# Kernel tuning notes

Measured on AMD Instinct MI355X. Metric: run time of the kernel, lower is better.

The kernel has to match this reference:

```python
import jax, jax.numpy as jnp
import numpy as np

GRID = 24          # sqrt(576)
MM = 1024          # mm_hidden_size
HID = 4096         # hidden_size
HEADS = 8          # mm_hidden_size // 128
NQ = GRID * GRID   # 576 queries / tokens
BATCH = 16
K = 2              # top-k == num_experts == 2


def _sincos_1d(d, pos):
    omega = np.arange(d // 2, dtype=np.float32) / (d / 2.0)
    omega = 1.0 / 10000 ** omega
    out = np.einsum('m,d->md', pos.reshape(-1).astype(np.float32), omega)
    return np.concatenate([np.sin(out), np.cos(out)], axis=1)


def _sincos_2d(d, g):
    gw, gh = np.meshgrid(np.arange(g, dtype=np.float32), np.arange(g, dtype=np.float32))
    return np.concatenate([_sincos_1d(d // 2, gh), _sincos_1d(d // 2, gw)], axis=1)


def layer_norm(x, g, b, eps=1e-5):
    mu = x.mean(-1, keepdims=True)
    var = ((x - mu) ** 2).mean(-1, keepdims=True)
    return (x - mu) * jax.lax.rsqrt(var + eps) * g + b


def mha(q, k, v, Wi, bi, Wo, bo, H):
    # q,k,v: [N, S, D]; Wi: [3D, D]; torch nn.MultiheadAttention semantics
    N, S, D = q.shape
    dh = D // H
    Wq, Wk, Wv = Wi[:D], Wi[D:2 * D], Wi[2 * D:]
    bq, bk, bv = bi[:D], bi[D:2 * D], bi[2 * D:]
    qp = (q @ Wq.T + bq).reshape(N, S, H, dh)
    kp = (k @ Wk.T + bk).reshape(N, -1, H, dh)
    vp = (v @ Wv.T + bv).reshape(N, -1, H, dh)
    scale = jnp.asarray(1.0 / np.sqrt(dh), q.dtype)
    scores = jnp.einsum('bqhd,bkhd->bhqk', qp, kp) * scale
    attn = jax.nn.softmax(scores, axis=-1)
    out = jnp.einsum('bhqk,bkhd->bqhd', attn, vp).reshape(N, S, D)
    return out @ Wo.T + bo


def _gating(xf, w_gate, w_noise, noise):
    # noisy top-k gating, training mode, k == num_experts == 2
    clean = xf @ w_gate                               # [B, 2]
    std = jax.nn.softplus(xf @ w_noise) + 0.01
    logits = jax.nn.softmax(clean + noise * std, axis=1)
    top_vals, top_idx = jax.lax.top_k(logits, K)      # min(k+1, n) == 2
    gates_k = top_vals / (top_vals.sum(1, keepdims=True) + 1e-6)
    rows = jnp.arange(xf.shape[0])[:, None]
    return jnp.zeros_like(logits).at[rows, top_idx].set(gates_k)


def setup_inputs() -> dict:
    key = jax.random.key(0)
    ks = jax.random.split(key, 10)
    s = 0.02
    f32 = jnp.float32
    return dict(
        x=jax.random.normal(ks[0], (BATCH, NQ, MM), f32),
        noise=jax.random.normal(ks[1], (BATCH * NQ, 2), f32),
        W1=jax.random.normal(ks[2], (HID, MM), f32) * s,
        b1=jnp.zeros((HID,), f32),
        W2=jax.random.normal(ks[3], (HID, HID), f32) * s,
        b2=jnp.zeros((HID,), f32),
        query=jax.random.normal(ks[4], (NQ, MM), f32) * s,
        pos_embed=jnp.asarray(_sincos_2d(MM, GRID), f32),
        ln_q_g=jnp.ones((MM,), f32), ln_q_b=jnp.zeros((MM,), f32),
        ln_kv_g=jnp.ones((MM,), f32), ln_kv_b=jnp.zeros((MM,), f32),
        in_proj_w=jax.random.normal(ks[5], (3 * MM, MM), f32) * s,
        in_proj_b=jnp.zeros((3 * MM,), f32),
        out_w=jax.random.normal(ks[6], (MM, MM), f32) * s,
        out_b=jnp.zeros((MM,), f32),
        w_gate=jax.random.normal(ks[7], (MM, 2), f32) * s,
        w_noise=jax.random.normal(ks[8], (MM, 2), f32) * s,
    )


def reference(x, noise, W1, b1, W2, b2, query, pos_embed, ln_q_g, ln_q_b,
              ln_kv_g, ln_kv_b, in_proj_w, in_proj_b, out_w, out_b,
              w_gate, w_noise):
    N, C, D = x.shape

    def projection(t):  # Linear -> GELU(exact) -> Linear
        h = jax.nn.gelu(t @ W1.T + b1, approximate=False)
        return h @ W2.T + b2

    # --- Resampler expert (kv_proj/ln_post/proj are identity here) ---
    kv = layer_norm(x, ln_kv_g, ln_kv_b)                    # [N, 576, D]
    q = layer_norm(query, ln_q_g, ln_q_b) + pos_embed       # [576, D]
    q = jnp.broadcast_to(q, (N, C, D))
    attn_out = mha(q, kv + pos_embed, kv, in_proj_w, in_proj_b, out_w, out_b, HEADS)

    e0 = projection(x)          # expert 0: MLP projection
    e1 = projection(attn_out)   # expert 1: resampler then projection

    gates = _gating(x.reshape(N * C, D), w_gate, w_noise, noise).reshape(N, C, 2)
    # stack(...,-1) @ gates[...,None] squeezed == gated sum over experts
    return e0 * gates[..., 0:1] + e1 * gates[..., 1:2]
```

## Files before the change

### kernel.cpp

```cpp
#include <hip/hip_runtime.h>
#include <hip/hip_bf16.h>
#include <cstdint>
#include <cstddef>

typedef __bf16 bf16;
typedef __bf16 bf16x4 __attribute__((ext_vector_type(4)));
typedef __bf16 bf16x8 __attribute__((ext_vector_type(8)));
typedef float  f32x4  __attribute__((ext_vector_type(4)));

#define BATCH 16
#define NQ    576
#define MM    1024
#define HID   4096
#define HEADS 8
#define DH    128
#define ROWS  (BATCH*NQ)

typedef const unsigned int __attribute__((address_space(1)))* gas_ptr;
typedef unsigned int __attribute__((address_space(3)))* las_ptr;

__device__ __forceinline__ void async16(const bf16* g, bf16* l) {
  __builtin_amdgcn_global_load_lds((gas_ptr)g, (las_ptr)l, 16, 0, 0);
}

__global__ __launch_bounds__(256) void cvt_kernel(
    const float* __restrict__ s, bf16* __restrict__ d)
{
  const int i = (blockIdx.x * 256 + threadIdx.x) * 4;
  f32x4 v = *(const f32x4*)(s + i);
  bf16x4 o;
#pragma unroll
  for (int j = 0; j < 4; ++j) o[j] = (bf16)v[j];
  *(bf16x4*)(d + i) = o;
}

enum { MODE_BIAS = 0, MODE_GG = 1, MODE_GGACC = 2, MODE_GB = 3 };

template <int MODE, typename OutT>
__global__ __launch_bounds__(256) void gemm_bt(
    const bf16* __restrict__ A, const bf16* __restrict__ W,
    const float* __restrict__ bias, OutT* __restrict__ C,
    const float* __restrict__ gates, int M, int N, int K)
{
  __shared__ bf16 As[128 * 32];
  __shared__ bf16 Bs[128 * 32];

  const int tid  = threadIdx.x;
  const int lane = tid & 63;
  const int w    = tid >> 6;
  const int wm   = (w & 1) * 64;
  const int wn   = (w >> 1) * 64;
  const int l15  = lane & 15;
  const int quad = lane >> 4;
  const int m0   = blockIdx.y * 128;
  const int n0   = blockIdx.x * 128;

  f32x4 acc[4][4] = {};

  int ar0 = m0 + (tid >> 2);      if (ar0 > M - 1) ar0 = M - 1;
  int ar1 = m0 + 64 + (tid >> 2); if (ar1 > M - 1) ar1 = M - 1;
  const int kc = (tid & 3) * 8;
  const bf16* ap0 = A + (size_t)ar0 * K + kc;
  const bf16* ap1 = A + (size_t)ar1 * K + kc;
  const bf16* bp0 = W + (size_t)(n0 + (tid >> 2)) * K + kc;
  const bf16* bp1 = W + (size_t)(n0 + 64 + (tid >> 2)) * K + kc;
  bf16* lA0 = As + tid * 8;
  bf16* lA1 = As + 2048 + tid * 8;
  bf16* lB0 = Bs + tid * 8;
  bf16* lB1 = Bs + 2048 + tid * 8;

  const int ko = quad * 8;

  for (int kt = 0; kt < K; kt += 32) {
    async16(ap0 + kt, lA0);
    async16(ap1 + kt, lA1);
    async16(bp0 + kt, lB0);
    async16(bp1 + kt, lB1);
    __syncthreads();

    bf16x8 af[4], bfr[4];
#pragma unroll
    for (int i = 0; i < 4; ++i)
      af[i] = *(const bf16x8*)(As + (wm + i * 16 + l15) * 32 + ko);
#pragma unroll
    for (int i = 0; i < 4; ++i)
      bfr[i] = *(const bf16x8*)(Bs + (wn + i * 16 + l15) * 32 + ko);
#pragma unroll
    for (int mi = 0; mi < 4; ++mi)
#pragma unroll
      for (int ni = 0; ni < 4; ++ni)
        acc[mi][ni] = __builtin_amdgcn_mfma_f32_16x16x32_bf16(
            af[mi], bfr[ni], acc[mi][ni], 0, 0, 0);
    __syncthreads();
  }

#pragma unroll
  for (int ni = 0; ni < 4; ++ni) {
    const int col = n0 + wn + ni * 16 + l15;
    const float bv = bias[col];
#pragma unroll
    for (int mi = 0; mi < 4; ++mi) {
      const int rowb = m0 + wm + mi * 16 + quad * 4;
#pragma unroll
      for (int r = 0; r < 4; ++r) {
        const int gr = rowb + r;
        if (gr < M) {
          const size_t idx = (size_t)gr * N + col;
          if (MODE == MODE_GB) {
            C[idx] = (OutT)(acc[mi][ni][r] +
                            (gates[gr * 2] + gates[gr * 2 + 1]) * bv);
          } else {
            float v = acc[mi][ni][r] + bv;
            if (MODE == MODE_GG || MODE == MODE_GGACC)
              v = 0.5f * v * (1.0f + erff(v * 0.70710678118654752f));
            if (MODE == MODE_GG)
              C[idx] = (OutT)(v * gates[gr * 2]);
            else if (MODE == MODE_GGACC)
              C[idx] = (OutT)((float)C[idx] + v * gates[gr * 2 + 1]);
            else
              C[idx] = (OutT)v;
          }
        }
      }
    }
  }
}

__global__ __launch_bounds__(256) void attn_kernel(
    const bf16* __restrict__ qp, const bf16* __restrict__ kp,
    const bf16* __restrict__ vp, bf16* __restrict__ ctx)
{
  __shared__ bf16 Qs[64 * 128];
  __shared__ bf16 Ks[64 * 128];
  __shared__ bf16 Vt[128 * 64];
  __shared__ bf16 Ps[64 * 64];

  const int qt = blockIdx.x, b = blockIdx.y, h = blockIdx.z;
  const int tid = threadIdx.x, lane = tid & 63, w = tid >> 6;
  const int l15 = lane & 15, quad = lane >> 4;
  const int q0 = qt * 64;

#pragma unroll
  for (int i = 0; i < 4; ++i) {
    const int c = i * 256 + tid;
    const int row = c >> 4, col = (c & 15) * 8;
    *(bf16x8*)(Qs + row * 128 + col) =
        *(const bf16x8*)(qp + (size_t)(q0 + row) * MM + h * DH + col);
  }

  float m_r[4], l_r[4];
  f32x4 accO[8] = {};
#pragma unroll
  for (int r = 0; r < 4; ++r) { m_r[r] = -1e30f; l_r[r] = 0.f; }

  const float scale = 0.08838834764831843f;

  for (int kt = 0; kt < 9; ++kt) {
    __syncthreads();
    const int kbase = b * NQ + kt * 64;
#pragma unroll
    for (int i = 0; i < 4; ++i) {
      const int c = i * 256 + tid;
      const int row = c >> 4, col = (c & 15) * 8;
      *(bf16x8*)(Ks + row * 128 + col) =
          *(const bf16x8*)(kp + (size_t)(kbase + row) * MM + h * DH + col);
      bf16x8 vv = *(const bf16x8*)(vp + (size_t)(kbase + row) * MM + h * DH + col);
#pragma unroll
      for (int j = 0; j < 8; ++j) Vt[(col + j) * 64 + row] = vv[j];
    }
    __syncthreads();

    f32x4 sacc[4] = {};
#pragma unroll
    for (int kcq = 0; kcq < 4; ++kcq) {
      bf16x8 aq = *(const bf16x8*)(Qs + (w * 16 + l15) * 128 + kcq * 32 + quad * 8);
#pragma unroll
      for (int ni = 0; ni < 4; ++ni) {
        bf16x8 bk = *(const bf16x8*)(Ks + (ni * 16 + l15) * 128 + kcq * 32 + quad * 8);
        sacc[ni] = __builtin_amdgcn_mfma_f32_16x16x32_bf16(aq, bk, sacc[ni], 0, 0, 0);
      }
    }
#pragma unroll
    for (int ni = 0; ni < 4; ++ni)
#pragma unroll
      for (int r = 0; r < 4; ++r) sacc[ni][r] *= scale;

    float p[4][4];
#pragma unroll
    for (int r = 0; r < 4; ++r) {
      float mx = fmaxf(fmaxf(sacc[0][r], sacc[1][r]), fmaxf(sacc[2][r], sacc[3][r]));
#pragma unroll
      for (int off = 8; off >= 1; off >>= 1) mx = fmaxf(mx, __shfl_xor(mx, off, 64));
      const float mnew = fmaxf(m_r[r], mx);
      const float al = expf(m_r[r] - mnew);
      float rs = 0.f;
#pragma unroll
      for (int ni = 0; ni < 4; ++ni) { p[ni][r] = expf(sacc[ni][r] - mnew); rs += p[ni][r]; }
#pragma unroll
      for (int off = 8; off >= 1; off >>= 1) rs += __shfl_xor(rs, off, 64);
      l_r[r] = l_r[r] * al + rs;
      m_r[r] = mnew;
#pragma unroll
      for (int ni2 = 0; ni2 < 8; ++ni2) accO[ni2][r] *= al;
    }

#pragma unroll
    for (int ni = 0; ni < 4; ++ni)
#pragma unroll
      for (int r = 0; r < 4; ++r)
        Ps[(w * 16 + quad * 4 + r) * 64 + ni * 16 + l15] = (bf16)p[ni][r];

#pragma unroll
    for (int kc2 = 0; kc2 < 2; ++kc2) {
      bf16x8 ap = *(const bf16x8*)(Ps + (w * 16 + l15) * 64 + kc2 * 32 + quad * 8);
#pragma unroll
      for (int ni2 = 0; ni2 < 8; ++ni2) {
        bf16x8 bv = *(const bf16x8*)(Vt + (ni2 * 16 + l15) * 64 + kc2 * 32 + quad * 8);
        accO[ni2] = __builtin_amdgcn_mfma_f32_16x16x32_bf16(ap, bv, accO[ni2], 0, 0, 0);
      }
    }
  }

#pragma unroll
  for (int r = 0; r < 4; ++r) {
    const float inv = 1.0f / l_r[r];
    const int qrow = q0 + w * 16 + quad * 4 + r;
#pragma unroll
    for (int ni2 = 0; ni2 < 8; ++ni2)
      ctx[(size_t)(b * NQ + qrow) * MM + h * DH + ni2 * 16 + l15] =
          (bf16)(accO[ni2][r] * inv);
  }
}

__global__ __launch_bounds__(256) void ln_kv_kernel(
    const float* __restrict__ x, const float* __restrict__ g,
    const float* __restrict__ bta, const float* __restrict__ pos,
    bf16* __restrict__ kv, bf16* __restrict__ kin)
{
  const int row = blockIdx.x, tid = threadIdx.x;
  f32x4 xv = *(const f32x4*)(x + (size_t)row * MM + tid * 4);
  float s = 0.f, ss = 0.f;
#pragma unroll
  for (int j = 0; j < 4; ++j) { s += xv[j]; ss += xv[j] * xv[j]; }
#pragma unroll
  for (int off = 32; off >= 1; off >>= 1) { s += __shfl_xor(s, off, 64); ss += __shfl_xor(ss, off, 64); }
  __shared__ float red[8];
  const int w = tid >> 6;
  if ((tid & 63) == 0) { red[w] = s; red[4 + w] = ss; }
  __syncthreads();
  s  = red[0] + red[1] + red[2] + red[3];
  ss = red[4] + red[5] + red[6] + red[7];
  const float mu = s * (1.0f / MM);
  const float rsig = rsqrtf(ss * (1.0f / MM) - mu * mu + 1e-5f);
  const int prow = row % NQ;
#pragma unroll
  for (int j = 0; j < 4; ++j) {
    const int c = tid * 4 + j;
    const float y = (xv[j] - mu) * rsig * g[c] + bta[c];
    kv[(size_t)row * MM + c]  = (bf16)y;
    kin[(size_t)row * MM + c] = (bf16)(y + pos[(size_t)prow * MM + c]);
  }
}

__global__ __launch_bounds__(256) void ln_q_kernel(
    const float* __restrict__ query, const float* __restrict__ g,
    const float* __restrict__ bta, const float* __restrict__ pos,
    bf16* __restrict__ qout)
{
  const int row = blockIdx.x, tid = threadIdx.x;
  f32x4 xv = *(const f32x4*)(query + (size_t)row * MM + tid * 4);
  float s = 0.f, ss = 0.f;
#pragma unroll
  for (int j = 0; j < 4; ++j) { s += xv[j]; ss += xv[j] * xv[j]; }
#pragma unroll
  for (int off = 32; off >= 1; off >>= 1) { s += __shfl_xor(s, off, 64); ss += __shfl_xor(ss, off, 64); }
  __shared__ float red[8];
  const int w = tid >> 6;
  if ((tid & 63) == 0) { red[w] = s; red[4 + w] = ss; }
  __syncthreads();
  s  = red[0] + red[1] + red[2] + red[3];
  ss = red[4] + red[5] + red[6] + red[7];
  const float mu = s * (1.0f / MM);
  const float rsig = rsqrtf(ss * (1.0f / MM) - mu * mu + 1e-5f);
#pragma unroll
  for (int j = 0; j < 4; ++j) {
    const int c = tid * 4 + j;
    const float y = (xv[j] - mu) * rsig * g[c] + bta[c] + pos[(size_t)row * MM + c];
    qout[(size_t)row * MM + c] = (bf16)y;
  }
}

__global__ __launch_bounds__(256) void gating_kernel(
    const float* __restrict__ x, const float* __restrict__ wg,
    const float* __restrict__ wn, const float* __restrict__ noise,
    float* __restrict__ gates)
{
  const int row = blockIdx.x, tid = threadIdx.x;
  f32x4 xv = *(const f32x4*)(x + (size_t)row * MM + tid * 4);
  float a0 = 0, a1 = 0, c0 = 0, c1 = 0;
#pragma unroll
  for (int j = 0; j < 4; ++j) {
    const int c = tid * 4 + j;
    a0 += xv[j] * wg[c * 2];
    a1 += xv[j] * wg[c * 2 + 1];
    c0 += xv[j] * wn[c * 2];
    c1 += xv[j] * wn[c * 2 + 1];
  }
#pragma unroll
  for (int off = 32; off >= 1; off >>= 1) {
    a0 += __shfl_xor(a0, off, 64); a1 += __shfl_xor(a1, off, 64);
    c0 += __shfl_xor(c0, off, 64); c1 += __shfl_xor(c1, off, 64);
  }
  __shared__ float red[16];
  const int w = tid >> 6;
  if ((tid & 63) == 0) { red[w * 4] = a0; red[w * 4 + 1] = a1; red[w * 4 + 2] = c0; red[w * 4 + 3] = c1; }
  __syncthreads();
  if (tid == 0) {
    a0 = red[0] + red[4] + red[8] + red[12];
    a1 = red[1] + red[5] + red[9] + red[13];
    c0 = red[2] + red[6] + red[10] + red[14];
    c1 = red[3] + red[7] + red[11] + red[15];
    const float sp0 = fmaxf(c0, 0.f) + log1pf(expf(-fabsf(c0)));
    const float sp1 = fmaxf(c1, 0.f) + log1pf(expf(-fabsf(c1)));
    const float l0 = a0 + noise[row * 2]     * (sp0 + 0.01f);
    const float l1 = a1 + noise[row * 2 + 1] * (sp1 + 0.01f);
    const float mx = fmaxf(l0, l1);
    const float e0 = expf(l0 - mx), e1 = expf(l1 - mx);
    const float inv = 1.0f / (e0 + e1);
    const float p0 = e0 * inv, p1 = e1 * inv;
    const float den = 1.0f / (p0 + p1 + 1e-6f);
    gates[row * 2]     = p0 * den;
    gates[row * 2 + 1] = p1 * den;
  }
}

extern "C" void kernel_launch(void* const* d_in, const int* in_sizes, int n_in,
                              void* d_out, int out_size, void* d_ws, size_t ws_size,
                              hipStream_t stream)
{
  const float* x       = (const float*)d_in[0];
  const float* noise   = (const float*)d_in[1];
  const float* W1      = (const float*)d_in[2];
  const float* b1      = (const float*)d_in[3];
  const float* W2      = (const float*)d_in[4];
  const float* b2      = (const float*)d_in[5];
  const float* query   = (const float*)d_in[6];
  const float* pos     = (const float*)d_in[7];
  const float* ln_q_g  = (const float*)d_in[8];
  const float* ln_q_b  = (const float*)d_in[9];
  const float* ln_kv_g = (const float*)d_in[10];
  const float* ln_kv_b = (const float*)d_in[11];
  const float* ipw     = (const float*)d_in[12];
  const float* ipb     = (const float*)d_in[13];
  const float* out_w   = (const float*)d_in[14];
  const float* out_b   = (const float*)d_in[15];
  const float* w_gate  = (const float*)d_in[16];
  const float* w_noise = (const float*)d_in[17];
  float* out = (float*)d_out;

  char* ws = (char*)d_ws;
  bf16*  kin   = (bf16*)(ws);
  bf16*  ctx   = kin;
  bf16*  kp    = (bf16*)(ws + 18874368);
  bf16*  vp    = (bf16*)(ws + 37748736);
  bf16*  qbuf  = (bf16*)(ws + 56623104);
  bf16*  qp    = (bf16*)(ws + 57802752);
  bf16*  ipwb  = (bf16*)(ws + 58982400);
  bf16*  outwb = (bf16*)(ws + 65273856);
  bf16*  h     = (bf16*)(ws);
  bf16*  x_bf  = (bf16*)(ws + 75497472);
  bf16*  W1b   = (bf16*)(ws + 94371840);
  bf16*  W2b   = (bf16*)(ws + 102760448);
  float* gates = (float*)(ws + 136314880);
  bf16*  kv       = (bf16*)d_out;
  bf16*  attn_out = (bf16*)((char*)d_out + 18874368);

  gating_kernel<<<ROWS, 256, 0, stream>>>(x, w_gate, w_noise, noise, gates);
  cvt_kernel<<<9216,  256, 0, stream>>>(x,  x_bf);
  cvt_kernel<<<4096,  256, 0, stream>>>(W1, W1b);
  cvt_kernel<<<16384, 256, 0, stream>>>(W2, W2b);
  cvt_kernel<<<3072,  256, 0, stream>>>(ipw,   ipwb);
  cvt_kernel<<<1024,  256, 0, stream>>>(out_w, outwb);

  ln_kv_kernel<<<ROWS, 256, 0, stream>>>(x, ln_kv_g, ln_kv_b, pos, kv, kin);
  ln_q_kernel<<<NQ, 256, 0, stream>>>(query, ln_q_g, ln_q_b, pos, qbuf);

  gemm_bt<MODE_BIAS, bf16><<<dim3(8, 5),  256, 0, stream>>>(qbuf, ipwb, ipb, qp, nullptr, NQ, MM, MM);
  gemm_bt<MODE_BIAS, bf16><<<dim3(8, 72), 256, 0, stream>>>(kin, ipwb + (size_t)MM * MM, ipb + MM, kp, nullptr, ROWS, MM, MM);
  gemm_bt<MODE_BIAS, bf16><<<dim3(8, 72), 256, 0, stream>>>(kv, ipwb + (size_t)2 * MM * MM, ipb + 2 * MM, vp, nullptr, ROWS, MM, MM);

  attn_kernel<<<dim3(9, BATCH, HEADS), 256, 0, stream>>>(qp, kp, vp, ctx);

  gemm_bt<MODE_BIAS, bf16><<<dim3(8, 72), 256, 0, stream>>>(ctx, outwb, out_b, attn_out, nullptr, ROWS, MM, MM);

  gemm_bt<MODE_GG,    bf16><<<dim3(32, 72), 256, 0, stream>>>(x_bf,     W1b, b1, h, gates, ROWS, HID, MM);
  gemm_bt<MODE_GGACC, bf16><<<dim3(32, 72), 256, 0, stream>>>(attn_out, W1b, b1, h, gates, ROWS, HID, MM);
  gemm_bt<MODE_GB,   float><<<dim3(32, 72), 256, 0, stream>>>(h,        W2b, b2, out, gates, ROWS, HID, HID);
}
```

Before: 1.413 ms.

## Add 256x256-tile triple-buffered GEMM kernel for the large projection GEMMs

Adds a new 512-thread GEMM kernel with 256x256 output tiles and a three-stage async global-to-LDS pipeline with XOR-swizzled shared memory. It also remaps workgroups in a swizzled order for cache locality and raises MFMA wave priority around the compute sections. The three large W1/W2 GEMMs now use it, while the old kernel is reduced to bias-only mode. The larger tiles are meant to raise arithmetic intensity and overlap loads with MFMA work, at the cost of more registers and LDS per block, lower occupancy, and no bounds checks, so M and N must be multiples of 256.

```diff
diff --git a/kernel.cpp b/kernel.cpp
--- a/kernel.cpp
+++ b/kernel.cpp
@@ -35,6 +35,143 @@
 }
 
 enum { MODE_BIAS = 0, MODE_GG = 1, MODE_GGACC = 2, MODE_GB = 3 };
+
+template <int MODE, typename OutT>
+__global__ __launch_bounds__(512) void gemm_big(
+    const bf16* __restrict__ A, const bf16* __restrict__ W,
+    const float* __restrict__ bias, OutT* __restrict__ C,
+    const float* __restrict__ gates, int M, int N, int K)
+{
+  __shared__ char LDS[3 * 32768];
+
+  const int tid  = threadIdx.x;
+  const int lane = tid & 63;
+  const int w    = tid >> 6;
+  const int w_m  = w >> 2;
+  const int w_n  = w & 3;
+  const int l15  = lane & 15;
+  const int quad = lane >> 4;
+
+  const int nwg = gridDim.x;
+  const int cpx = nwg >> 3;
+  const int sw  = (blockIdx.x & 7) * cpx + (blockIdx.x >> 3);
+  const int ntn = N >> 8;
+  const int m0  = (sw / ntn) << 8;
+  const int n0  = (sw % ntn) << 8;
+
+  const int srow   = tid >> 2;
+  const int schunk = (tid & 3) ^ (srow & 3);
+  const bf16* aS0 = A + (size_t)(m0 + srow) * K + schunk * 8;
+  const bf16* bS0 = W + (size_t)(n0 + srow) * K + schunk * 8;
+  const size_t rowskip = (size_t)128 * K;
+
+  const int axor  = (quad ^ (l15 & 3)) << 4;
+  const int abase = (w_m * 128 + l15) * 64 + axor;
+  const int bbase = 16384 + (w_n * 64 + l15) * 64 + axor;
+
+  f32x4 acc[8][4] = {};
+  const int nt = K >> 5;
+
+  {
+    char* s0 = LDS;
+    async16(aS0,            (bf16*)(s0 + tid * 16));
+    async16(aS0 + rowskip,  (bf16*)(s0 + 8192  + tid * 16));
+    async16(bS0,            (bf16*)(s0 + 16384 + tid * 16));
+    async16(bS0 + rowskip,  (bf16*)(s0 + 24576 + tid * 16));
+    char* s1 = LDS + 32768;
+    const bf16* a1 = aS0 + 32;
+    const bf16* b1 = bS0 + 32;
+    async16(a1,             (bf16*)(s1 + tid * 16));
+    async16(a1 + rowskip,   (bf16*)(s1 + 8192  + tid * 16));
+    async16(b1,             (bf16*)(s1 + 16384 + tid * 16));
+    async16(b1 + rowskip,   (bf16*)(s1 + 24576 + tid * 16));
+  }
+  asm volatile("s_waitcnt vmcnt(4)" ::: "memory");
+  __builtin_amdgcn_sched_barrier(0);
+  __builtin_amdgcn_s_barrier();
+
+  for (int t = 0; t < nt; ++t) {
+    char* cs = LDS + (t % 3) * 32768;
+    char* ps = LDS + ((t + 2) % 3) * 32768;
+    const bool pf = (t + 2 < nt);
+
+    bf16x8 af[8], bfr[4];
+#pragma unroll
+    for (int i = 0; i < 4; ++i)
+      af[i] = *(const bf16x8*)(cs + abase + i * 1024);
+#pragma unroll
+    for (int i = 0; i < 4; ++i)
+      bfr[i] = *(const bf16x8*)(cs + bbase + i * 1024);
+    if (pf) {
+      const bf16* _a = aS0 + (size_t)(t + 2) * 32;
+      async16(_a,           (bf16*)(ps + tid * 16));
+      async16(_a + rowskip, (bf16*)(ps + 8192 + tid * 16));
+    }
+    __builtin_amdgcn_s_barrier();
+    __builtin_amdgcn_s_setprio(1);
+#pragma unroll
+    for (int mi = 0; mi < 4; ++mi)
+#pragma unroll
+      for (int ni = 0; ni < 4; ++ni)
+        acc[mi][ni] = __builtin_amdgcn_mfma_f32_16x16x32_bf16(
+            af[mi], bfr[ni], acc[mi][ni], 0, 0, 0);
+    __builtin_amdgcn_s_setprio(0);
+    __builtin_amdgcn_s_barrier();
+
+#pragma unroll
+    for (int i = 4; i < 8; ++i)
+      af[i] = *(const bf16x8*)(cs + abase + i * 1024);
+    if (pf) {
+      const bf16* _b = bS0 + (size_t)(t + 2) * 32;
+      async16(_b,           (bf16*)(ps + 16384 + tid * 16));
+      async16(_b + rowskip, (bf16*)(ps + 24576 + tid * 16));
+      asm volatile("s_waitcnt vmcnt(4)" ::: "memory");
+      __builtin_amdgcn_sched_barrier(0);
+    } else if (t + 1 < nt) {
+      asm volatile("s_waitcnt vmcnt(0)" ::: "memory");
+      __builtin_amdgcn_sched_barrier(0);
+    }
+    __builtin_amdgcn_s_barrier();
+    __builtin_amdgcn_s_setprio(1);
+#pragma unroll
+    for (int mi = 4; mi < 8; ++mi)
+#pragma unroll
+      for (int ni = 0; ni < 4; ++ni)
+        acc[mi][ni] = __builtin_amdgcn_mfma_f32_16x16x32_bf16(
+            af[mi], bfr[ni], acc[mi][ni], 0, 0, 0);
+    __builtin_amdgcn_s_setprio(0);
+    __builtin_amdgcn_s_barrier();
+  }
+
+#pragma unroll
+  for (int ni = 0; ni < 4; ++ni) {
+    const int col = n0 + w_n * 64 + ni * 16 + l15;
+    const float bv = bias[col];
+#pragma unroll
+    for (int mi = 0; mi < 8; ++mi) {
+      const int rowb = m0 + w_m * 128 + mi * 16 + quad * 4;
+#pragma unroll
+      for (int r = 0; r < 4; ++r) {
+        const int gr = rowb + r;
+        const size_t idx = (size_t)gr * N + col;
+        if (MODE == MODE_GB) {
+          C[idx] = (OutT)(acc[mi][ni][r] +
+                          (gates[gr * 2] + gates[gr * 2 + 1]) * bv);
+        } else {
+          float v = acc[mi][ni][r] + bv;
+          if (MODE == MODE_GG || MODE == MODE_GGACC)
+            v = 0.5f * v * (1.0f + erff(v * 0.70710678118654752f));
+          if (MODE == MODE_GG)
+            C[idx] = (OutT)(v * gates[gr * 2]);
+          else if (MODE == MODE_GGACC)
+            C[idx] = (OutT)((float)C[idx] + v * gates[gr * 2 + 1]);
+          else
+            C[idx] = (OutT)v;
+        }
+      }
+    }
+  }
+}
 
 template <int MODE, typename OutT>
 __global__ __launch_bounds__(256) void gemm_bt(
@@ -106,20 +243,8 @@
         const int gr = rowb + r;
         if (gr < M) {
           const size_t idx = (size_t)gr * N + col;
-          if (MODE == MODE_GB) {
-            C[idx] = (OutT)(acc[mi][ni][r] +
-                            (gates[gr * 2] + gates[gr * 2 + 1]) * bv);
-          } else {
-            float v = acc[mi][ni][r] + bv;
-            if (MODE == MODE_GG || MODE == MODE_GGACC)
-              v = 0.5f * v * (1.0f + erff(v * 0.70710678118654752f));
-            if (MODE == MODE_GG)
-              C[idx] = (OutT)(v * gates[gr * 2]);
-            else if (MODE == MODE_GGACC)
-              C[idx] = (OutT)((float)C[idx] + v * gates[gr * 2 + 1]);
-            else
-              C[idx] = (OutT)v;
-          }
+          float v = acc[mi][ni][r] + bv;
+          C[idx] = (OutT)v;
         }
       }
     }
@@ -393,7 +518,7 @@
 
   gemm_bt<MODE_BIAS, bf16><<<dim3(8, 72), 256, 0, stream>>>(ctx, outwb, out_b, attn_out, nullptr, ROWS, MM, MM);
 
-  gemm_bt<MODE_GG,    bf16><<<dim3(32, 72), 256, 0, stream>>>(x_bf,     W1b, b1, h, gates, ROWS, HID, MM);
-  gemm_bt<MODE_GGACC, bf16><<<dim3(32, 72), 256, 0, stream>>>(attn_out, W1b, b1, h, gates, ROWS, HID, MM);
-  gemm_bt<MODE_GB,   float><<<dim3(32, 72), 256, 0, stream>>>(h,        W2b, b2, out, gates, ROWS, HID, HID);
-}
+  gemm_big<MODE_GG,    bf16><<<576, 512, 0, stream>>>(x_bf,     W1b, b1, h, gates, ROWS, HID, MM);
+  gemm_big<MODE_GGACC, bf16><<<576, 512, 0, stream>>>(attn_out, W1b, b1, h, gates, ROWS, HID, MM);
+  gemm_big<MODE_GB,   float><<<576, 512, 0, stream>>>(h,        W2b, b2, out, gates, ROWS, HID, HID);
+}
```

Result: slower. 1.464 ms (+3.6%).

## Fuse both W1 expert GEMMs into one dual-accumulator kernel, add XCD-aware block remap

Applied to the files above, without the earlier changes.

The two first-layer projection GEMMs (x and attn_out against W1) are merged into one kernel that loads each W1 tile once and keeps two accumulator sets. GELU and the gated sum are applied in the epilogue, which removes the read-modify-write of h between the two launches and halves the W1 tile traffic. Every GEMM also remaps its block index so that consecutive tiles land on the same XCD, which should improve L2 reuse. The price is twice the accumulator registers (128 fp32 per lane), which may lower occupancy or cause spills.

```diff
diff --git a/kernel.cpp b/kernel.cpp
--- a/kernel.cpp
+++ b/kernel.cpp
@@ -34,7 +34,7 @@
   *(bf16x4*)(d + i) = o;
 }
 
-enum { MODE_BIAS = 0, MODE_GG = 1, MODE_GGACC = 2, MODE_GB = 3 };
+enum { MODE_BIAS = 0, MODE_GB = 3 };
 
 template <int MODE, typename OutT>
 __global__ __launch_bounds__(256) void gemm_bt(
@@ -52,8 +52,14 @@
   const int wn   = (w >> 1) * 64;
   const int l15  = lane & 15;
   const int quad = lane >> 4;
-  const int m0   = blockIdx.y * 128;
-  const int n0   = blockIdx.x * 128;
+
+  const int gx  = gridDim.x;
+  const int nwg = gx * gridDim.y;
+  const int cpx = nwg >> 3;
+  int lin = blockIdx.y * gx + blockIdx.x;
+  lin = (lin & 7) * cpx + (lin >> 3);
+  const int m0 = (lin / gx) * 128;
+  const int n0 = (lin % gx) * 128;
 
   f32x4 acc[4][4] = {};
 
@@ -106,21 +112,110 @@
         const int gr = rowb + r;
         if (gr < M) {
           const size_t idx = (size_t)gr * N + col;
-          if (MODE == MODE_GB) {
+          if (MODE == MODE_GB)
             C[idx] = (OutT)(acc[mi][ni][r] +
                             (gates[gr * 2] + gates[gr * 2 + 1]) * bv);
-          } else {
-            float v = acc[mi][ni][r] + bv;
-            if (MODE == MODE_GG || MODE == MODE_GGACC)
-              v = 0.5f * v * (1.0f + erff(v * 0.70710678118654752f));
-            if (MODE == MODE_GG)
-              C[idx] = (OutT)(v * gates[gr * 2]);
-            else if (MODE == MODE_GGACC)
-              C[idx] = (OutT)((float)C[idx] + v * gates[gr * 2 + 1]);
-            else
-              C[idx] = (OutT)v;
-          }
+          else
+            C[idx] = (OutT)(acc[mi][ni][r] + bv);
         }
+      }
+    }
+  }
+}
+
+__global__ __launch_bounds__(256) void gemm_w1d(
+    const bf16* __restrict__ X, const bf16* __restrict__ A2,
+    const bf16* __restrict__ W, const float* __restrict__ b1v,
+    bf16* __restrict__ H, const float* __restrict__ gates,
+    int M, int N, int K)
+{
+  __shared__ bf16 Xs[128 * 32];
+  __shared__ bf16 Zs[128 * 32];
+  __shared__ bf16 Ws[128 * 32];
+
+  const int tid  = threadIdx.x;
+  const int lane = tid & 63;
+  const int w    = tid >> 6;
+  const int wm   = (w & 1) * 64;
+  const int wn   = (w >> 1) * 64;
+  const int l15  = lane & 15;
+  const int quad = lane >> 4;
+
+  const int gx  = gridDim.x;
+  const int nwg = gx * gridDim.y;
+  const int cpx = nwg >> 3;
+  int lin = blockIdx.y * gx + blockIdx.x;
+  lin = (lin & 7) * cpx + (lin >> 3);
+  const int m0 = (lin / gx) * 128;
+  const int n0 = (lin % gx) * 128;
+
+  const int sr = tid >> 2;
+  const int kc = (tid & 3) * 8;
+  const bf16* xp0 = X  + (size_t)(m0 + sr) * K + kc;
+  const bf16* xp1 = xp0 + (size_t)64 * K;
+  const bf16* zp0 = A2 + (size_t)(m0 + sr) * K + kc;
+  const bf16* zp1 = zp0 + (size_t)64 * K;
+  const bf16* wp0 = W  + (size_t)(n0 + sr) * K + kc;
+  const bf16* wp1 = wp0 + (size_t)64 * K;
+  bf16* lX0 = Xs + tid * 8;
+  bf16* lX1 = Xs + 2048 + tid * 8;
+  bf16* lZ0 = Zs + tid * 8;
+  bf16* lZ1 = Zs + 2048 + tid * 8;
+  bf16* lW0 = Ws + tid * 8;
+  bf16* lW1 = Ws + 2048 + tid * 8;
+
+  const int ko = quad * 8;
+
+  f32x4 ax[4][4] = {};
+  f32x4 az[4][4] = {};
+
+  for (int kt = 0; kt < K; kt += 32) {
+    async16(xp0 + kt, lX0);
+    async16(xp1 + kt, lX1);
+    async16(zp0 + kt, lZ0);
+    async16(zp1 + kt, lZ1);
+    async16(wp0 + kt, lW0);
+    async16(wp1 + kt, lW1);
+    __syncthreads();
+
+    bf16x8 xf[4], zf[4], wf[4];
+#pragma unroll
+    for (int i = 0; i < 4; ++i)
+      xf[i] = *(const bf16x8*)(Xs + (wm + i * 16 + l15) * 32 + ko);
+#pragma unroll
+    for (int i = 0; i < 4; ++i)
+      zf[i] = *(const bf16x8*)(Zs + (wm + i * 16 + l15) * 32 + ko);
+#pragma unroll
+    for (int i = 0; i < 4; ++i)
+      wf[i] = *(const bf16x8*)(Ws + (wn + i * 16 + l15) * 32 + ko);
+#pragma unroll
+    for (int mi = 0; mi < 4; ++mi)
+#pragma unroll
+      for (int ni = 0; ni < 4; ++ni) {
+        ax[mi][ni] = __builtin_amdgcn_mfma_f32_16x16x32_bf16(
+            xf[mi], wf[ni], ax[mi][ni], 0, 0, 0);
+        az[mi][ni] = __builtin_amdgcn_mfma_f32_16x16x32_bf16(
+            zf[mi], wf[ni], az[mi][ni], 0, 0, 0);
+      }
+    __syncthreads();
+  }
+
+#pragma unroll
+  for (int ni = 0; ni < 4; ++ni) {
+    const int col = n0 + wn + ni * 16 + l15;
+    const float bv = b1v[col];
+#pragma unroll
+    for (int mi = 0; mi < 4; ++mi) {
+      const int rowb = m0 + wm + mi * 16 + quad * 4;
+#pragma unroll
+      for (int r = 0; r < 4; ++r) {
+        const int gr = rowb + r;
+        float vx = ax[mi][ni][r] + bv;
+        vx = 0.5f * vx * (1.0f + erff(vx * 0.70710678118654752f));
+        float vz = az[mi][ni][r] + bv;
+        vz = 0.5f * vz * (1.0f + erff(vz * 0.70710678118654752f));
+        H[(size_t)gr * N + col] =
+            (bf16)(vx * gates[gr * 2] + vz * gates[gr * 2 + 1]);
       }
     }
   }
@@ -393,7 +488,6 @@
 
   gemm_bt<MODE_BIAS, bf16><<<dim3(8, 72), 256, 0, stream>>>(ctx, outwb, out_b, attn_out, nullptr, ROWS, MM, MM);
 
-  gemm_bt<MODE_GG,    bf16><<<dim3(32, 72), 256, 0, stream>>>(x_bf,     W1b, b1, h, gates, ROWS, HID, MM);
-  gemm_bt<MODE_GGACC, bf16><<<dim3(32, 72), 256, 0, stream>>>(attn_out, W1b, b1, h, gates, ROWS, HID, MM);
-  gemm_bt<MODE_GB,   float><<<dim3(32, 72), 256, 0, stream>>>(h,        W2b, b2, out, gates, ROWS, HID, HID);
-}
+  gemm_w1d<<<dim3(32, 72), 256, 0, stream>>>(x_bf, attn_out, W1b, b1, h, gates, ROWS, HID, MM);
+  gemm_bt<MODE_GB, float><<<dim3(32, 72), 256, 0, stream>>>(h, W2b, b2, out, gates, ROWS, HID, HID);
+}
```

After: 1.595 ms. 1.13x slower.
